# Optimization experiments

Measured on AMD Instinct MI355X. Metric: run time of the kernel, lower is better.

## Reference

```python
import jax, jax.numpy as jnp
import numpy as np

S, B, H = 4096, 64, 256
D = 2.0
SIGMA = D / 2.0


def setup_inputs() -> dict:
    key = jax.random.key(0)
    ks = jax.random.split(key, 7)
    return {
        "e": jax.random.normal(ks[0], (S, B, H), dtype=jnp.float32),
        "d": jax.random.normal(ks[1], (1, B, H), dtype=jnp.float32),
        "W_a": jax.random.normal(ks[2], (H, H), dtype=jnp.float32) / np.sqrt(H),
        "W_p": jax.random.normal(ks[3], (H, H), dtype=jnp.float32) / np.sqrt(H),
        "v_p": jax.random.normal(ks[4], (H, 1), dtype=jnp.float32) / np.sqrt(H),
        "lin_w": jax.random.normal(ks[5], (H, 2 * H), dtype=jnp.float32) / np.sqrt(2 * H),
        "lin_b": jax.random.normal(ks[6], (H,), dtype=jnp.float32) * 0.01,
    }


def reference(e, d, W_a, W_p, v_p, lin_w, lin_b):
    s = e.shape[0]
    # alignment: scores over source positions, softmax along S (dim 0 in torch)
    scores = jnp.sum((d @ W_a) * e, axis=2)          # [S, B]
    a = jax.nn.softmax(scores, axis=0)               # [S, B]
    # predictive position gating (Luong local-p attention)
    h = jnp.tanh(d[0] @ W_p)                         # [B, H]
    p_center = jax.nn.sigmoid((h @ v_p)[:, 0])[None, :] * s   # [1, B]
    pos = jnp.arange(s, dtype=e.dtype)[:, None]      # [S, 1]
    diff = p_center - pos                            # [S, B]
    mask = (jnp.abs(diff) <= D).astype(e.dtype)
    p = jnp.exp(-(diff * diff) / (2.0 * SIGMA * SIGMA)) * mask  # [S, B]
    w = a * p                                        # [S, B]
    context = jnp.einsum('sbh,sb->bh', e, w)[None]   # [1, B, H]
    x = jnp.concatenate([context, d], axis=2)        # [1, B, 2H]
    out = jax.nn.relu(x @ lin_w.T + lin_b)           # dropout = identity (eval)
    return out, w
```

## Files before the change

### kernel.cpp

```cpp
#include <hip/hip_runtime.h>
#include <math.h>

constexpr int S_ = 4096;
constexpr int B_ = 64;
constexpr int H_ = 256;


__global__ __launch_bounds__(256) void k1_prep(const float* __restrict__ d,
                                               const float* __restrict__ W_a,
                                               const float* __restrict__ W_p,
                                               const float* __restrict__ v_p,
                                               float* __restrict__ dW,
                                               float* __restrict__ pc) {
  int b = blockIdx.x;
  int h = threadIdx.x;
  float acc_a = 0.f, acc_p = 0.f;
  const float* db = d + b * H_;
  for (int k = 0; k < H_; ++k) {
    float dv = db[k];
    acc_a = fmaf(dv, W_a[k * H_ + h], acc_a);
    acc_p = fmaf(dv, W_p[k * H_ + h], acc_p);
  }
  dW[b * H_ + h] = acc_a;
  float prod = tanhf(acc_p) * v_p[h];
  __shared__ float red[256];
  red[h] = prod;
  __syncthreads();
  for (int st = 128; st > 0; st >>= 1) {
    if (h < st) red[h] += red[h + st];
    __syncthreads();
  }
  if (h == 0) {
    pc[b] = (float)S_ / (1.f + expf(-red[0]));
  }
}

__global__ __launch_bounds__(256) void k2_scores(const float* __restrict__ e,
                                                 const float* __restrict__ dW,
                                                 float* __restrict__ scores) {
  int b = blockIdx.y;
  int wave = threadIdx.x >> 6;
  int lane = threadIdx.x & 63;
  float4 wv = *(const float4*)(dW + b * H_ + lane * 4);
  int s_base = blockIdx.x * 64 + wave * 16;
  const float* ebase = e + (size_t)b * H_ + (size_t)lane * 4;
  for (int i = 0; i < 16; ++i) {
    int s = s_base + i;
    const float4 ev = *(const float4*)(ebase + (size_t)s * (B_ * H_));
    float acc = fmaf(ev.x, wv.x, fmaf(ev.y, wv.y, fmaf(ev.z, wv.z, ev.w * wv.w)));
#pragma unroll
    for (int off = 32; off > 0; off >>= 1) acc += __shfl_xor(acc, off, 64);
    if (lane == 0) scores[b * S_ + s] = acc;
  }
}

__global__ __launch_bounds__(256) void k3a_stats(const float* __restrict__ scores,
                                                 float* __restrict__ m,
                                                 float* __restrict__ l) {
  int b = blockIdx.x;
  int t = threadIdx.x;
  const float* sc = scores + b * S_;
  float v[16];
  float lm = -INFINITY;
#pragma unroll
  for (int k = 0; k < 16; ++k) {
    v[k] = sc[t + k * 256];
    lm = fmaxf(lm, v[k]);
  }
  __shared__ float red[256];
  red[t] = lm;
  __syncthreads();
  for (int st = 128; st > 0; st >>= 1) {
    if (t < st) red[t] = fmaxf(red[t], red[t + st]);
    __syncthreads();
  }
  float mb = red[0];
  __syncthreads();
  float ls = 0.f;
#pragma unroll
  for (int k = 0; k < 16; ++k) ls += expf(v[k] - mb);
  red[t] = ls;
  __syncthreads();
  for (int st = 128; st > 0; st >>= 1) {
    if (t < st) red[t] += red[t + st];
    __syncthreads();
  }
  if (t == 0) { m[b] = mb; l[b] = red[0]; }
}

__global__ __launch_bounds__(256) void k3b_weights(const float* __restrict__ scores,
                                                   const float* __restrict__ m,
                                                   const float* __restrict__ l,
                                                   const float* __restrict__ pc,
                                                   float* __restrict__ w_out) {
  __shared__ float tile[64][65];
  int t = threadIdx.x;
  int s0 = blockIdx.x * 64;
#pragma unroll
  for (int k = 0; k < 16; ++k) {
    int idx = t + k * 256;
    int b = idx >> 6;
    int sl = idx & 63;
    int s = s0 + sl;
    float a = expf(scores[b * S_ + s] - m[b]) / l[b];
    float diff = pc[b] - (float)s;
    float p = (fabsf(diff) <= 2.f) ? expf(-0.5f * diff * diff) : 0.f;
    tile[b][sl] = a * p;
  }
  __syncthreads();
#pragma unroll
  for (int k = 0; k < 16; ++k) {
    int idx = t + k * 256;
    int sl = idx >> 6;
    int b = idx & 63;
    w_out[(size_t)(s0 + sl) * B_ + b] = tile[b][sl];
  }
}

__global__ __launch_bounds__(256) void k4_out(const float* __restrict__ e,
                                              const float* __restrict__ d,
                                              const float* __restrict__ lin_w,
                                              const float* __restrict__ lin_b,
                                              const float* __restrict__ pc,
                                              const float* __restrict__ w_out,
                                              float* __restrict__ out) {
  int b = blockIdx.x;
  int h = threadIdx.x;
  float pcb = pc[b];
  int s0 = max(0, (int)ceilf(pcb - 2.f));
  int s1 = min(S_ - 1, (int)floorf(pcb + 2.f));
  float ctx = 0.f;
  for (int s = s0; s <= s1; ++s) {
    float wv = w_out[(size_t)s * B_ + b];
    ctx = fmaf(wv, e[((size_t)s * B_ + b) * H_ + h], ctx);
  }
  __shared__ float x[512];
  x[h] = ctx;
  x[256 + h] = d[b * H_ + h];
  __syncthreads();
  float acc = lin_b[h];
  const float4* lw = (const float4*)(lin_w + h * 2 * H_);
  const float4* xv = (const float4*)x;
#pragma unroll 4
  for (int k = 0; k < 128; ++k) {
    float4 a4 = lw[k];
    float4 b4 = xv[k];
    acc += a4.x * b4.x + a4.y * b4.y + a4.z * b4.z + a4.w * b4.w;
  }
  out[b * H_ + h] = fmaxf(acc, 0.f);
}

extern "C" void kernel_launch(void* const* d_in, const int* in_sizes, int n_in,
                              void* d_out, int out_size, void* d_ws, size_t ws_size,
                              hipStream_t stream) {
  const float* e     = (const float*)d_in[0];
  const float* d     = (const float*)d_in[1];
  const float* W_a   = (const float*)d_in[2];
  const float* W_p   = (const float*)d_in[3];
  const float* v_p   = (const float*)d_in[4];
  const float* lin_w = (const float*)d_in[5];
  const float* lin_b = (const float*)d_in[6];

  float* out   = (float*)d_out;
  float* w_out = out + B_ * H_;

  float* ws     = (float*)d_ws;
  float* dW     = ws;
  float* pc     = ws + 16384;
  float* m      = ws + 16448;
  float* l      = ws + 16512;
  float* scores = ws + 16576;

  k1_prep<<<B_, 256, 0, stream>>>(d, W_a, W_p, v_p, dW, pc);
  k2_scores<<<dim3(S_ / 64, B_), 256, 0, stream>>>(e, dW, scores);
  k3a_stats<<<B_, 256, 0, stream>>>(scores, m, l);
  k3b_weights<<<S_ / 64, 256, 0, stream>>>(scores, m, l, pc, w_out);
  k4_out<<<B_, 256, 0, stream>>>(e, d, lin_w, lin_b, pc, w_out, out);
}
```

Measured before the change: 84.38 us.

## Fuse softmax stats, weight write and output projection into one kernel

Merges the softmax-statistics, weight-computation and output kernels into a single per-batch kernel. It recomputes the few local-window weights in registers instead of rereading them from global memory, which removes two launches and the m/l and w round trips. The scores grid is reordered so consecutive blocks cover different batches, and e loads are batched eight at a time to raise memory-level parallelism. The cost is that w_out is now written with a strided pattern (stride B) from only 64 blocks, which may coalesce worse than the old transposed-tile write.

```diff
diff --git a/kernel.cpp b/kernel.cpp
--- a/kernel.cpp
+++ b/kernel.cpp
@@ -38,25 +38,36 @@
 __global__ __launch_bounds__(256) void k2_scores(const float* __restrict__ e,
                                                  const float* __restrict__ dW,
                                                  float* __restrict__ scores) {
-  int b = blockIdx.y;
+  int b = blockIdx.x;
   int wave = threadIdx.x >> 6;
   int lane = threadIdx.x & 63;
   float4 wv = *(const float4*)(dW + b * H_ + lane * 4);
-  int s_base = blockIdx.x * 64 + wave * 16;
-  const float* ebase = e + (size_t)b * H_ + (size_t)lane * 4;
-  for (int i = 0; i < 16; ++i) {
-    int s = s_base + i;
-    const float4 ev = *(const float4*)(ebase + (size_t)s * (B_ * H_));
-    float acc = fmaf(ev.x, wv.x, fmaf(ev.y, wv.y, fmaf(ev.z, wv.z, ev.w * wv.w)));
+  int s_base = blockIdx.y * 64 + wave * 16;
+  const float* ebase = e + (size_t)s_base * (B_ * H_) + (size_t)b * H_ + (size_t)lane * 4;
+#pragma unroll 1
+  for (int c = 0; c < 2; ++c) {
+    float4 ev[8];
 #pragma unroll
-    for (int off = 32; off > 0; off >>= 1) acc += __shfl_xor(acc, off, 64);
-    if (lane == 0) scores[b * S_ + s] = acc;
+    for (int i = 0; i < 8; ++i)
+      ev[i] = *(const float4*)(ebase + (size_t)(c * 8 + i) * (B_ * H_));
+#pragma unroll
+    for (int i = 0; i < 8; ++i) {
+      float acc = fmaf(ev[i].x, wv.x, fmaf(ev[i].y, wv.y, fmaf(ev[i].z, wv.z, ev[i].w * wv.w)));
+#pragma unroll
+      for (int off = 32; off > 0; off >>= 1) acc += __shfl_xor(acc, off, 64);
+      if (lane == 0) scores[b * S_ + s_base + c * 8 + i] = acc;
+    }
   }
 }
 
-__global__ __launch_bounds__(256) void k3a_stats(const float* __restrict__ scores,
-                                                 float* __restrict__ m,
-                                                 float* __restrict__ l) {
+__global__ __launch_bounds__(256) void kF(const float* __restrict__ scores,
+                                          const float* __restrict__ pc,
+                                          const float* __restrict__ e,
+                                          const float* __restrict__ d,
+                                          const float* __restrict__ lin_w,
+                                          const float* __restrict__ lin_b,
+                                          float* __restrict__ out,
+                                          float* __restrict__ w_out) {
   int b = blockIdx.x;
   int t = threadIdx.x;
   const float* sc = scores + b * S_;
@@ -85,61 +96,29 @@
     if (t < st) red[t] += red[t + st];
     __syncthreads();
   }
-  if (t == 0) { m[b] = mb; l[b] = red[0]; }
-}
-
-__global__ __launch_bounds__(256) void k3b_weights(const float* __restrict__ scores,
-                                                   const float* __restrict__ m,
-                                                   const float* __restrict__ l,
-                                                   const float* __restrict__ pc,
-                                                   float* __restrict__ w_out) {
-  __shared__ float tile[64][65];
-  int t = threadIdx.x;
-  int s0 = blockIdx.x * 64;
+  float inv_l = 1.f / red[0];
+  float pcb = pc[b];
 #pragma unroll
   for (int k = 0; k < 16; ++k) {
-    int idx = t + k * 256;
-    int b = idx >> 6;
-    int sl = idx & 63;
-    int s = s0 + sl;
-    float a = expf(scores[b * S_ + s] - m[b]) / l[b];
-    float diff = pc[b] - (float)s;
+    int s = t + k * 256;
+    float diff = pcb - (float)s;
     float p = (fabsf(diff) <= 2.f) ? expf(-0.5f * diff * diff) : 0.f;
-    tile[b][sl] = a * p;
+    w_out[(size_t)s * B_ + b] = expf(v[k] - mb) * inv_l * p;
   }
-  __syncthreads();
-#pragma unroll
-  for (int k = 0; k < 16; ++k) {
-    int idx = t + k * 256;
-    int sl = idx >> 6;
-    int b = idx & 63;
-    w_out[(size_t)(s0 + sl) * B_ + b] = tile[b][sl];
-  }
-}
-
-__global__ __launch_bounds__(256) void k4_out(const float* __restrict__ e,
-                                              const float* __restrict__ d,
-                                              const float* __restrict__ lin_w,
-                                              const float* __restrict__ lin_b,
-                                              const float* __restrict__ pc,
-                                              const float* __restrict__ w_out,
-                                              float* __restrict__ out) {
-  int b = blockIdx.x;
-  int h = threadIdx.x;
-  float pcb = pc[b];
   int s0 = max(0, (int)ceilf(pcb - 2.f));
   int s1 = min(S_ - 1, (int)floorf(pcb + 2.f));
   float ctx = 0.f;
   for (int s = s0; s <= s1; ++s) {
-    float wv = w_out[(size_t)s * B_ + b];
-    ctx = fmaf(wv, e[((size_t)s * B_ + b) * H_ + h], ctx);
+    float diff = pcb - (float)s;
+    float wv = expf(sc[s] - mb) * inv_l * expf(-0.5f * diff * diff);
+    ctx = fmaf(wv, e[((size_t)s * B_ + b) * H_ + t], ctx);
   }
   __shared__ float x[512];
-  x[h] = ctx;
-  x[256 + h] = d[b * H_ + h];
+  x[t] = ctx;
+  x[256 + t] = d[b * H_ + t];
   __syncthreads();
-  float acc = lin_b[h];
-  const float4* lw = (const float4*)(lin_w + h * 2 * H_);
+  float acc = lin_b[t];
+  const float4* lw = (const float4*)(lin_w + t * 2 * H_);
   const float4* xv = (const float4*)x;
 #pragma unroll 4
   for (int k = 0; k < 128; ++k) {
@@ -147,7 +126,7 @@
     float4 b4 = xv[k];
     acc += a4.x * b4.x + a4.y * b4.y + a4.z * b4.z + a4.w * b4.w;
   }
-  out[b * H_ + h] = fmaxf(acc, 0.f);
+  out[b * H_ + t] = fmaxf(acc, 0.f);
 }
 
 extern "C" void kernel_launch(void* const* d_in, const int* in_sizes, int n_in,
@@ -167,13 +146,9 @@
   float* ws     = (float*)d_ws;
   float* dW     = ws;
   float* pc     = ws + 16384;
-  float* m      = ws + 16448;
-  float* l      = ws + 16512;
-  float* scores = ws + 16576;
+  float* scores = ws + 16448;
 
   k1_prep<<<B_, 256, 0, stream>>>(d, W_a, W_p, v_p, dW, pc);
-  k2_scores<<<dim3(S_ / 64, B_), 256, 0, stream>>>(e, dW, scores);
-  k3a_stats<<<B_, 256, 0, stream>>>(scores, m, l);
-  k3b_weights<<<S_ / 64, 256, 0, stream>>>(scores, m, l, pc, w_out);
-  k4_out<<<B_, 256, 0, stream>>>(e, d, lin_w, lin_b, pc, w_out, out);
+  k2_scores<<<dim3(B_, S_ / 64), 256, 0, stream>>>(e, dW, scores);
+  kF<<<B_, 256, 0, stream>>>(scores, pc, e, d, lin_w, lin_b, out, w_out);
 }
```

Measured after the change: 83.87 us. No clear change (-0.6%).
